# Kernel optimization log

Measured on AMD Instinct MI355X. Metric: run time of the kernel, lower is better.

The kernel has to match this reference:

```python
import jax, jax.numpy as jnp
import numpy as np

VOCAB, EDIM, WFEAT, LABELS, SLOPE = 50000, 128, 128, 2, 0.01
N = 8192

def setup_inputs() -> dict:
    key = jax.random.key(0)
    ks = jax.random.split(key, 8)
    inSen = jax.random.randint(ks[0], (N,), 0, VOCAB, dtype=jnp.int64) if jax.config.read('jax_enable_x64') else jax.random.randint(ks[0], (N,), 0, VOCAB, dtype=jnp.int32)
    adj = jax.random.randint(ks[1], (N, N), 0, 2, dtype=jnp.int32)
    emb = jax.random.normal(ks[2], (VOCAB, EDIM), dtype=jnp.float32)
    W = jax.random.normal(ks[3], (EDIM, WFEAT), dtype=jnp.float32) * (1.0 / np.sqrt(EDIM))
    a_src = jax.random.normal(ks[4], (WFEAT,), dtype=jnp.float32) * (1.0 / np.sqrt(WFEAT))
    a_dst = jax.random.normal(ks[5], (WFEAT,), dtype=jnp.float32) * (1.0 / np.sqrt(WFEAT))
    cls_W = jax.random.normal(ks[6], (WFEAT, LABELS), dtype=jnp.float32) * (1.0 / np.sqrt(WFEAT))
    cls_b = jax.random.normal(ks[7], (LABELS,), dtype=jnp.float32) * 0.01
    return {"inSen": inSen, "adj": adj, "selfLink": 1, "emb": emb, "W": W,
            "a_src": a_src, "a_dst": a_dst, "cls_W": cls_W, "cls_b": cls_b}

def reference(inSen, adj, selfLink, emb, W, a_src, a_dst, cls_W, cls_b):
    # Embedding lookup: (N, edim)
    words = emb[inSen]
    # GAT layer: linear projection then adjacency-masked additive attention
    h = words @ W                              # (N, wFeat)
    f_src = h @ a_src                          # (N,)
    f_dst = h @ a_dst                          # (N,)
    e = jax.nn.leaky_relu(f_src[:, None] + f_dst[None, :], negative_slope=SLOPE)  # (N, N)
    mask = (adj + selfLink * jnp.eye(adj.shape[0], dtype=adj.dtype)) > 0
    e = jnp.where(mask, e, jnp.float32(-1e9))
    attention = jax.nn.softmax(e, axis=1)      # (N, N)
    sentence = attention @ h                   # (N, wFeat)
    # Max pool over words, classify
    poolSentence = jnp.max(sentence, axis=0)   # (wFeat,)
    label = jax.nn.softmax(poolSentence @ cls_W + cls_b, axis=0)  # (labels,)
    return (poolSentence, attention, sentence, label)
```

## Files before the change

kernel.cpp:

```cpp
#include <hip/hip_runtime.h>
#include <hip/hip_bf16.h>

#define NR 8192
#define WF 128

typedef short bf16x8 __attribute__((ext_vector_type(8)));
typedef float f32x4 __attribute__((ext_vector_type(4)));

static __device__ __forceinline__ unsigned int f2bf(float f) {
    unsigned int u = __float_as_uint(f);
    return (u + 0x7fffu + ((u >> 16) & 1u)) >> 16;
}
static __device__ __forceinline__ void atomicMaxF(float* addr, float v) {
    if (v >= 0.f) atomicMax((int*)addr, __float_as_int(v));
    else          atomicMin((unsigned int*)addr, __float_as_uint(v));
}
static __device__ __forceinline__ float lrelu(float x) { return x > 0.f ? x : 0.01f * x; }

__global__ __launch_bounds__(256) void k_proj(
    const int* __restrict__ inSen, const float* __restrict__ emb,
    const float* __restrict__ W, const float* __restrict__ a_src,
    const float* __restrict__ a_dst, float* __restrict__ f_src,
    float* __restrict__ f_dst, float* __restrict__ maxfd,
    unsigned short* __restrict__ hB)
{
    __shared__ float ht[16 * 132];
    const int t = threadIdx.x;
    const int f = t & 127, rh = t >> 7;
    const int i0 = blockIdx.x * 16;

    int wd[8];
    #pragma unroll
    for (int r = 0; r < 8; ++r) wd[r] = inSen[i0 + rh * 8 + r];
    float h[8];
    #pragma unroll
    for (int r = 0; r < 8; ++r) h[r] = 0.f;

    for (int k4 = 0; k4 < 32; ++k4) {
        const float w0 = W[(k4 * 4 + 0) * WF + f];
        const float w1 = W[(k4 * 4 + 1) * WF + f];
        const float w2 = W[(k4 * 4 + 2) * WF + f];
        const float w3 = W[(k4 * 4 + 3) * WF + f];
        #pragma unroll
        for (int r = 0; r < 8; ++r) {
            float4 ev = ((const float4*)(emb + (size_t)wd[r] * 128))[k4];
            h[r] += ev.x * w0 + ev.y * w1 + ev.z * w2 + ev.w * w3;
        }
    }
    #pragma unroll
    for (int r = 0; r < 8; ++r) ht[(rh * 8 + r) * 132 + f] = h[r];
    __syncthreads();

    if (t < 16) {
        float s = 0.f, d = 0.f;
        for (int k4 = 0; k4 < 32; ++k4) {
            float4 hv = *(const float4*)(ht + t * 132 + k4 * 4);
            float4 as = ((const float4*)a_src)[k4];
            float4 ad = ((const float4*)a_dst)[k4];
            s += hv.x * as.x + hv.y * as.y + hv.z * as.z + hv.w * as.w;
            d += hv.x * ad.x + hv.y * ad.y + hv.z * ad.z + hv.w * ad.w;
        }
        f_src[i0 + t] = s;
        f_dst[i0 + t] = d;
        float dm = d;
        #pragma unroll
        for (int o = 1; o < 16; o <<= 1) dm = fmaxf(dm, __shfl_xor(dm, o));
        if (t == 0) atomicMaxF(maxfd, dm);
    }
    {
        const int kb = blockIdx.x >> 1, half = blockIdx.x & 1;
        const int nf = t >> 5, l32 = t & 31;
        const int qloc = l32 >> 4, fx = l32 & 15;
        const int lane = (half * 2 + qloc) * 16 + fx;
        const float* hp = ht + (qloc * 8) * 132 + nf * 16 + fx;
        uint4 v;
        v.x = f2bf(hp[0 * 132]) | (f2bf(hp[1 * 132]) << 16);
        v.y = f2bf(hp[2 * 132]) | (f2bf(hp[3 * 132]) << 16);
        v.z = f2bf(hp[4 * 132]) | (f2bf(hp[5 * 132]) << 16);
        v.w = f2bf(hp[6 * 132]) | (f2bf(hp[7 * 132]) << 16);
        *(uint4*)(hB + ((size_t)kb * 8 + nf) * 512 + lane * 8) = v;
    }
}

static __device__ __forceinline__ void adj_chunk(
    int c, int4 a, const float* __restrict__ fdl, int lane, int row, int sl,
    float fs, float C, int shl,
    unsigned int* __restrict__ mrow, float& sum)
{
    const float4 f = *(const float4*)(fdl + c * 256 + 4 * lane);
    const bool m0 = a.x > 0, m1 = a.y > 0, m2 = a.z > 0, m3 = a.w > 0;
    float p0 = m0 ? __expf(lrelu(fs + f.x) - C) : 0.f;
    float p1 = m1 ? __expf(lrelu(fs + f.y) - C) : 0.f;
    float p2 = m2 ? __expf(lrelu(fs + f.z) - C) : 0.f;
    float p3 = m3 ? __expf(lrelu(fs + f.w) - C) : 0.f;
    unsigned int nib = (m0 ? 1u : 0u) | (m1 ? 2u : 0u) | (m2 ? 4u : 0u) | (m3 ? 8u : 0u);
    float ssum = p0 + p1 + p2 + p3;
    if (c == (row >> 8)) {
        if (lane == ((row & 255) >> 2)) {
            const int jd = row & 3;
            const int aj = jd == 0 ? a.x : jd == 1 ? a.y : jd == 2 ? a.z : a.w;
            const float fj = jd == 0 ? f.x : jd == 1 ? f.y : jd == 2 ? f.z : f.w;
            const bool mo = aj > 0, mn = (aj + sl) > 0;
            if (mn != mo) {
                const float pd = __expf(lrelu(fs + fj) - C);
                if (mn) { nib |= 1u << jd; ssum += pd; }
                else    { nib &= ~(1u << jd); ssum -= pd; }
            }
        }
    }
    sum += ssum;
    unsigned int v = nib << shl;
    v |= __shfl_xor(v, 1);
    v |= __shfl_xor(v, 2);
    v |= __shfl_xor(v, 4);
    if ((lane & 7) == 0) mrow[c * 8 + (lane >> 3)] = v;
}

__global__ __launch_bounds__(256, 4) void k_adj(
    const int* __restrict__ adj, const int* __restrict__ slP,
    const float* __restrict__ f_src, const float* __restrict__ f_dst,
    const float* __restrict__ maxfd, unsigned int* __restrict__ maskG,
    float* __restrict__ invl)
{
    __shared__ float fdl[NR];
    const int t = threadIdx.x, lane = t & 63, w = t >> 6;
    const int row = blockIdx.x * 4 + w;
    const int sl = slP[0];
    const int* __restrict__ ap = adj + (size_t)row * NR + 4 * lane;

    int4 a0 = *(const int4*)(ap + 0 * 256);
    int4 a1 = *(const int4*)(ap + 1 * 256);
    int4 a2 = *(const int4*)(ap + 2 * 256);
    int4 a3 = *(const int4*)(ap + 3 * 256);
    int4 a4 = *(const int4*)(ap + 4 * 256);
    int4 a5 = *(const int4*)(ap + 5 * 256);
    int4 a6 = *(const int4*)(ap + 6 * 256);
    int4 a7 = *(const int4*)(ap + 7 * 256);

    #pragma unroll
    for (int i = 0; i < 8; ++i)
        *(float4*)(fdl + (i * 256 + t) * 4) = *(const float4*)(f_dst + (i * 256 + t) * 4);

    const float fs = f_src[row];
    const float C = lrelu(fs + maxfd[0]);
    unsigned int* __restrict__ mrow = maskG + (size_t)row * 256;
    const int shl = 4 * (lane & 7);
    float sum = 0.f;
    __syncthreads();

    #define ADJC(c, reg) adj_chunk((c), (reg), fdl, lane, row, sl, fs, C, shl, mrow, sum)
    #pragma unroll 1
    for (int g = 0; g < 24; g += 8) {
        ADJC(g + 0, a0); a0 = *(const int4*)(ap + (g +  8) * 256);
        ADJC(g + 1, a1); a1 = *(const int4*)(ap + (g +  9) * 256);
        ADJC(g + 2, a2); a2 = *(const int4*)(ap + (g + 10) * 256);
        ADJC(g + 3, a3); a3 = *(const int4*)(ap + (g + 11) * 256);
        ADJC(g + 4, a4); a4 = *(const int4*)(ap + (g + 12) * 256);
        ADJC(g + 5, a5); a5 = *(const int4*)(ap + (g + 13) * 256);
        ADJC(g + 6, a6); a6 = *(const int4*)(ap + (g + 14) * 256);
        ADJC(g + 7, a7); a7 = *(const int4*)(ap + (g + 15) * 256);
    }
    ADJC(24, a0); ADJC(25, a1); ADJC(26, a2); ADJC(27, a3);
    ADJC(28, a4); ADJC(29, a5); ADJC(30, a6); ADJC(31, a7);
    #undef ADJC

    #pragma unroll
    for (int o = 1; o < 64; o <<= 1) sum += __shfl_xor(sum, o);
    if (lane == 0) invl[row] = 1.0f / sum;
}

__global__ __launch_bounds__(512, 4) void k_att(
    const unsigned int* __restrict__ maskG, const float* __restrict__ f_src,
    const float* __restrict__ f_dst, const float* __restrict__ maxfd,
    const float* __restrict__ invl, const unsigned short* __restrict__ hB,
    float* __restrict__ att, float* __restrict__ sent, float* __restrict__ partial)
{
    __shared__ float red[8][2048];
    float* fdl = &red[0][0];
    const int t = threadIdx.x;
    const int lane = t & 63, w = t >> 6;
    const int strip = blockIdx.x;
    const int i0 = strip * 16;
    const int fx = lane & 15, quad = lane >> 4;
    const int row = i0 + fx;

    #pragma unroll
    for (int i = 0; i < 4; ++i)
        *(float4*)(fdl + (i * 512 + t) * 4) = *(const float4*)(f_dst + (i * 512 + t) * 4);

    const float fs = f_src[row];
    const float C = lrelu(fs + maxfd[0]);
    const float il = invl[row];
    float* __restrict__ ar = att + (size_t)row * NR;
    const unsigned int* __restrict__ mrow = maskG + (size_t)row * 256;
    f32x4 acc[8] = {};
    const int k0 = w * 1024;
    __syncthreads();

    for (int kk4 = k0; kk4 < k0 + 1024; kk4 += 128) {
        const uint4 mw = *(const uint4*)(mrow + (kk4 >> 5));
        const unsigned int mwa[4] = {mw.x, mw.y, mw.z, mw.w};
        #pragma unroll
        for (int j4 = 0; j4 < 4; ++j4) {
            const int kk = kk4 + j4 * 32;
            const int kb = kk >> 5;
            const unsigned short* hp = hB + (size_t)kb * 4096 + lane * 8;
            bf16x8 bfr[8];
            #pragma unroll
            for (int nf = 0; nf < 8; ++nf) bfr[nf] = *(const bf16x8*)(hp + nf * 512);

            const unsigned int mbyte = (mwa[j4] >> (quad * 8)) & 0xffu;
            const float4 fd0 = *(const float4*)(fdl + kk + quad * 8);
            const float4 fd1 = *(const float4*)(fdl + kk + quad * 8 + 4);
            const float fv[8] = {fd0.x, fd0.y, fd0.z, fd0.w, fd1.x, fd1.y, fd1.z, fd1.w};
            float p[8];
            #pragma unroll
            for (int j = 0; j < 8; ++j)
                p[j] = ((mbyte >> j) & 1u) ? __expf(lrelu(fs + fv[j]) - C) : 0.f;

            const float4 w0 = make_float4(p[0] * il, p[1] * il, p[2] * il, p[3] * il);
            const float4 w1 = make_float4(p[4] * il, p[5] * il, p[6] * il, p[7] * il);
            *(float4*)(ar + kk + quad * 8) = w0;
            *(float4*)(ar + kk + quad * 8 + 4) = w1;

            union { uint4 u; bf16x8 v; } cv;
            cv.u.x = f2bf(p[0]) | (f2bf(p[1]) << 16);
            cv.u.y = f2bf(p[2]) | (f2bf(p[3]) << 16);
            cv.u.z = f2bf(p[4]) | (f2bf(p[5]) << 16);
            cv.u.w = f2bf(p[6]) | (f2bf(p[7]) << 16);
            #pragma unroll
            for (int nf = 0; nf < 8; ++nf)
                acc[nf] = __builtin_amdgcn_mfma_f32_16x16x32_bf16(cv.v, bfr[nf], acc[nf], 0, 0, 0);
        }
    }
    __syncthreads();
    #pragma unroll
    for (int reg = 0; reg < 4; ++reg) {
        #pragma unroll
        for (int nf = 0; nf < 8; ++nf)
            red[w][(quad * 4 + reg) * 128 + nf * 16 + fx] = acc[nf][reg];
    }
    __syncthreads();
    const int e0 = t * 4;
    const int m = e0 >> 7, f0 = e0 & 127;
    {
        const float vin = invl[i0 + m];
        float vv[4];
        #pragma unroll
        for (int j = 0; j < 4; ++j) {
            float s = 0.f;
            #pragma unroll
            for (int sx = 0; sx < 8; ++sx) s += red[sx][e0 + j];
            vv[j] = s * vin;
        }
        *(float4*)(sent + (size_t)(i0 + m) * WF + f0) = make_float4(vv[0], vv[1], vv[2], vv[3]);
        red[0][e0 + 0] = vv[0]; red[0][e0 + 1] = vv[1];
        red[0][e0 + 2] = vv[2]; red[0][e0 + 3] = vv[3];
    }
    __syncthreads();
    if (t < 128) {
        float mx = red[0][t];
        #pragma unroll
        for (int mm = 1; mm < 16; ++mm) mx = fmaxf(mx, red[0][mm * 128 + t]);
        partial[strip * 128 + t] = mx;
    }
}

__global__ __launch_bounds__(128) void k_label(
    const float* __restrict__ partial, const float* __restrict__ cls_W,
    const float* __restrict__ cls_b, float* __restrict__ pool,
    float* __restrict__ label)
{
    __shared__ float s0[128], s1[128];
    const int t = threadIdx.x;
    float m0 = -1e30f, m1 = -1e30f, m2 = -1e30f, m3 = -1e30f;
    for (int b = 0; b < 512; b += 4) {
        m0 = fmaxf(m0, partial[(b + 0) * 128 + t]);
        m1 = fmaxf(m1, partial[(b + 1) * 128 + t]);
        m2 = fmaxf(m2, partial[(b + 2) * 128 + t]);
        m3 = fmaxf(m3, partial[(b + 3) * 128 + t]);
    }
    const float m = fmaxf(fmaxf(m0, m1), fmaxf(m2, m3));
    pool[t] = m;
    s0[t] = m * cls_W[t * 2 + 0];
    s1[t] = m * cls_W[t * 2 + 1];
    __syncthreads();
    if (t == 0) {
        float z0 = cls_b[0], z1 = cls_b[1];
        for (int f = 0; f < 128; ++f) { z0 += s0[f]; z1 += s1[f]; }
        float mm = fmaxf(z0, z1);
        float e0 = __expf(z0 - mm), e1 = __expf(z1 - mm);
        float inv = 1.0f / (e0 + e1);
        label[0] = e0 * inv;
        label[1] = e1 * inv;
    }
}

extern "C" void kernel_launch(void* const* d_in, const int* in_sizes, int n_in,
                              void* d_out, int out_size, void* d_ws, size_t ws_size,
                              hipStream_t stream)
{
    const int*   inSen    = (const int*)d_in[0];
    const int*   adj      = (const int*)d_in[1];
    const int*   selfLink = (const int*)d_in[2];
    const float* emb      = (const float*)d_in[3];
    const float* W        = (const float*)d_in[4];
    const float* a_src    = (const float*)d_in[5];
    const float* a_dst    = (const float*)d_in[6];
    const float* cls_W    = (const float*)d_in[7];
    const float* cls_b    = (const float*)d_in[8];

    float* out   = (float*)d_out;
    float* pool  = out;
    float* att   = out + 128;
    float* sent  = att + (size_t)NR * NR;
    float* label = sent + (size_t)NR * WF;

    char* ws = (char*)d_ws;
    unsigned short* hB    = (unsigned short*)ws;
    unsigned int*   maskG = (unsigned int*)(ws + (2u << 20));
    float* f_src   = (float*)(ws + (10u << 20));
    float* f_dst   = f_src + NR;
    float* invl    = f_dst + NR;
    float* maxfd   = invl + NR;
    float* partial = maxfd + 64;

    hipMemsetAsync(maxfd, 0xFF, 4, stream);
    k_proj<<<NR / 16, 256, 0, stream>>>(inSen, emb, W, a_src, a_dst, f_src, f_dst, maxfd, hB);
    k_adj<<<NR / 4, 256, 0, stream>>>(adj, selfLink, f_src, f_dst, maxfd, maskG, invl);
    k_att<<<NR / 16, 512, 0, stream>>>(maskG, f_src, f_dst, maxfd, invl, hB, att, sent, partial);
    k_label<<<1, 128, 0, stream>>>(partial, cls_W, cls_b, pool, label);
}
```

Baseline: 596.0 us.

## Fuse adjacency-mask pass into attention kernel, keeping bitmask and row sums in LDS

Merges the adjacency-scan kernel into the attention kernel. Each 512-thread block first scans its own 16 adj rows, two rows per wave, and writes the packed bitmask into padded shared memory along with the inverse row sums. The MFMA attention pass then reads the mask and sums from LDS instead of global memory. This removes a kernel launch and the global round trip of the mask and invl arrays. The cost is that the adj read is serialized with the compute phase inside each block, and the shared memory reuse of red[] for the mask may limit overlap.

New measurement: 585.8 us. About the same (-1.7%).

```diff
diff --git a/kernel.cpp b/kernel.cpp
--- a/kernel.cpp
+++ b/kernel.cpp
@@ -3,6 +3,7 @@
 
 #define NR 8192
 #define WF 128
+#define MSTRIDE 260
 
 typedef short bf16x8 __attribute__((ext_vector_type(8)));
 typedef float f32x4 __attribute__((ext_vector_type(4)));
@@ -116,38 +117,13 @@
     if ((lane & 7) == 0) mrow[c * 8 + (lane >> 3)] = v;
 }
 
-__global__ __launch_bounds__(256, 4) void k_adj(
-    const int* __restrict__ adj, const int* __restrict__ slP,
-    const float* __restrict__ f_src, const float* __restrict__ f_dst,
-    const float* __restrict__ maxfd, unsigned int* __restrict__ maskG,
-    float* __restrict__ invl)
-{
-    __shared__ float fdl[NR];
-    const int t = threadIdx.x, lane = t & 63, w = t >> 6;
-    const int row = blockIdx.x * 4 + w;
-    const int sl = slP[0];
-    const int* __restrict__ ap = adj + (size_t)row * NR + 4 * lane;
-
-    int4 a0 = *(const int4*)(ap + 0 * 256);
-    int4 a1 = *(const int4*)(ap + 1 * 256);
-    int4 a2 = *(const int4*)(ap + 2 * 256);
-    int4 a3 = *(const int4*)(ap + 3 * 256);
-    int4 a4 = *(const int4*)(ap + 4 * 256);
-    int4 a5 = *(const int4*)(ap + 5 * 256);
-    int4 a6 = *(const int4*)(ap + 6 * 256);
-    int4 a7 = *(const int4*)(ap + 7 * 256);
-
-    #pragma unroll
-    for (int i = 0; i < 8; ++i)
-        *(float4*)(fdl + (i * 256 + t) * 4) = *(const float4*)(f_dst + (i * 256 + t) * 4);
-
-    const float fs = f_src[row];
-    const float C = lrelu(fs + maxfd[0]);
-    unsigned int* __restrict__ mrow = maskG + (size_t)row * 256;
-    const int shl = 4 * (lane & 7);
+static __device__ __forceinline__ float adj_row(
+    const int* __restrict__ ap, const float* __restrict__ fdl,
+    int lane, int row, int sl, float fs, float C, int shl,
+    unsigned int* __restrict__ mrow,
+    int4 a0, int4 a1, int4 a2, int4 a3, int4 a4, int4 a5, int4 a6, int4 a7)
+{
     float sum = 0.f;
-    __syncthreads();
-
     #define ADJC(c, reg) adj_chunk((c), (reg), fdl, lane, row, sl, fs, C, shl, mrow, sum)
     #pragma unroll 1
     for (int g = 0; g < 24; g += 8) {
@@ -163,39 +139,82 @@
     ADJC(24, a0); ADJC(25, a1); ADJC(26, a2); ADJC(27, a3);
     ADJC(28, a4); ADJC(29, a5); ADJC(30, a6); ADJC(31, a7);
     #undef ADJC
-
-    #pragma unroll
-    for (int o = 1; o < 64; o <<= 1) sum += __shfl_xor(sum, o);
-    if (lane == 0) invl[row] = 1.0f / sum;
-}
-
-__global__ __launch_bounds__(512, 4) void k_att(
-    const unsigned int* __restrict__ maskG, const float* __restrict__ f_src,
-    const float* __restrict__ f_dst, const float* __restrict__ maxfd,
-    const float* __restrict__ invl, const unsigned short* __restrict__ hB,
+    return sum;
+}
+
+__global__ __launch_bounds__(512, 4) void k_fused(
+    const int* __restrict__ adj, const int* __restrict__ slP,
+    const float* __restrict__ f_src, const float* __restrict__ f_dst,
+    const float* __restrict__ maxfd, const unsigned short* __restrict__ hB,
     float* __restrict__ att, float* __restrict__ sent, float* __restrict__ partial)
 {
     __shared__ float red[8][2048];
+    __shared__ float sums[16];
     float* fdl = &red[0][0];
-    const int t = threadIdx.x;
-    const int lane = t & 63, w = t >> 6;
+    unsigned int* mask = (unsigned int*)&red[4][0];
+    const int t = threadIdx.x, lane = t & 63, w = t >> 6;
     const int strip = blockIdx.x;
     const int i0 = strip * 16;
+
+    const int rowA = i0 + 2 * w;
+    const int* __restrict__ apA = adj + (size_t)rowA * NR + 4 * lane;
+    int4 a0 = *(const int4*)(apA + 0 * 256);
+    int4 a1 = *(const int4*)(apA + 1 * 256);
+    int4 a2 = *(const int4*)(apA + 2 * 256);
+    int4 a3 = *(const int4*)(apA + 3 * 256);
+    int4 a4 = *(const int4*)(apA + 4 * 256);
+    int4 a5 = *(const int4*)(apA + 5 * 256);
+    int4 a6 = *(const int4*)(apA + 6 * 256);
+    int4 a7 = *(const int4*)(apA + 7 * 256);
+
+    #pragma unroll
+    for (int i = 0; i < 4; ++i)
+        *(float4*)(fdl + (i * 512 + t) * 4) = *(const float4*)(f_dst + (i * 512 + t) * 4);
+
+    const int sl = slP[0];
+    const float mfd = maxfd[0];
+    const int shl = 4 * (lane & 7);
+    __syncthreads();
+
+    {
+        const float fsA = f_src[rowA];
+        const float CA = lrelu(fsA + mfd);
+        float s = adj_row(apA, fdl, lane, rowA, sl, fsA, CA, shl,
+                          mask + (2 * w) * MSTRIDE, a0, a1, a2, a3, a4, a5, a6, a7);
+        #pragma unroll
+        for (int o = 1; o < 64; o <<= 1) s += __shfl_xor(s, o);
+        if (lane == 0) sums[2 * w] = 1.0f / s;
+    }
+    {
+        const int rowB = i0 + 2 * w + 1;
+        const int* __restrict__ apB = adj + (size_t)rowB * NR + 4 * lane;
+        int4 b0 = *(const int4*)(apB + 0 * 256);
+        int4 b1 = *(const int4*)(apB + 1 * 256);
+        int4 b2 = *(const int4*)(apB + 2 * 256);
+        int4 b3 = *(const int4*)(apB + 3 * 256);
+        int4 b4 = *(const int4*)(apB + 4 * 256);
+        int4 b5 = *(const int4*)(apB + 5 * 256);
+        int4 b6 = *(const int4*)(apB + 6 * 256);
+        int4 b7 = *(const int4*)(apB + 7 * 256);
+        const float fsB = f_src[rowB];
+        const float CB = lrelu(fsB + mfd);
+        float s = adj_row(apB, fdl, lane, rowB, sl, fsB, CB, shl,
+                          mask + (2 * w + 1) * MSTRIDE, b0, b1, b2, b3, b4, b5, b6, b7);
+        #pragma unroll
+        for (int o = 1; o < 64; o <<= 1) s += __shfl_xor(s, o);
+        if (lane == 0) sums[2 * w + 1] = 1.0f / s;
+    }
+    __syncthreads();
+
     const int fx = lane & 15, quad = lane >> 4;
     const int row = i0 + fx;
-
-    #pragma unroll
-    for (int i = 0; i < 4; ++i)
-        *(float4*)(fdl + (i * 512 + t) * 4) = *(const float4*)(f_dst + (i * 512 + t) * 4);
-
     const float fs = f_src[row];
-    const float C = lrelu(fs + maxfd[0]);
-    const float il = invl[row];
+    const float C = lrelu(fs + mfd);
+    const float il = sums[fx];
     float* __restrict__ ar = att + (size_t)row * NR;
-    const unsigned int* __restrict__ mrow = maskG + (size_t)row * 256;
+    const unsigned int* __restrict__ mrow = mask + fx * MSTRIDE;
     f32x4 acc[8] = {};
     const int k0 = w * 1024;
-    __syncthreads();
 
     for (int kk4 = k0; kk4 < k0 + 1024; kk4 += 128) {
         const uint4 mw = *(const uint4*)(mrow + (kk4 >> 5));
@@ -244,7 +263,7 @@
     const int e0 = t * 4;
     const int m = e0 >> 7, f0 = e0 & 127;
     {
-        const float vin = invl[i0 + m];
+        const float vin = sums[m];
         float vv[4];
         #pragma unroll
         for (int j = 0; j < 4; ++j) {
@@ -318,16 +337,13 @@
 
     char* ws = (char*)d_ws;
     unsigned short* hB    = (unsigned short*)ws;
-    unsigned int*   maskG = (unsigned int*)(ws + (2u << 20));
-    float* f_src   = (float*)(ws + (10u << 20));
+    float* f_src   = (float*)(ws + (2u << 20));
     float* f_dst   = f_src + NR;
-    float* invl    = f_dst + NR;
-    float* maxfd   = invl + NR;
+    float* maxfd   = f_dst + NR;
     float* partial = maxfd + 64;
 
     hipMemsetAsync(maxfd, 0xFF, 4, stream);
     k_proj<<<NR / 16, 256, 0, stream>>>(inSen, emb, W, a_src, a_dst, f_src, f_dst, maxfd, hB);
-    k_adj<<<NR / 4, 256, 0, stream>>>(adj, selfLink, f_src, f_dst, maxfd, maskG, invl);
-    k_att<<<NR / 16, 512, 0, stream>>>(maskG, f_src, f_dst, maxfd, invl, hB, att, sent, partial);
+    k_fused<<<NR / 16, 512, 0, stream>>>(adj, selfLink, f_src, f_dst, maxfd, hB, att, sent, partial);
     k_label<<<1, 128, 0, stream>>>(partial, cls_W, cls_b, pool, label);
 }
```
